# Performance work log

Measured on AMD Instinct MI355X. Metric: run time of the kernel, lower is better.

The kernel has to match this reference:

```python
import jax, jax.numpy as jnp
import numpy as np

N, E, H = 4096, 32768, 8
D0, C1, C2, C3 = 256, 448, 384, 256
K, M, G = 4, 500, 2000
NEG = 0.2   # GATConv LeakyReLU negative slope
EPS = 1e-5  # LayerNorm eps


def _gat(x, src, dst, W, a_s, a_d, b, heads, out_ch, concat):
    # PyG GATConv (self-loops already appended to src/dst by caller).
    n = x.shape[0]
    xp = (x @ W).reshape(n, heads, out_ch)                 # [N,H,C]
    s = jnp.einsum('nhc,hc->nh', xp, a_s)                  # alpha_src per node
    d = jnp.einsum('nhc,hc->nh', xp, a_d)                  # alpha_dst per node
    e = jax.nn.leaky_relu(s[src] + d[dst], NEG)            # [E,H]
    m = jax.ops.segment_max(e, dst, num_segments=n)
    m = jnp.where(jnp.isfinite(m), m, 0.0)
    p = jnp.exp(e - m[dst])
    z = jax.ops.segment_sum(p, dst, num_segments=n)
    alpha = p / (z[dst] + 1e-16)                           # per-dst softmax
    out = jax.ops.segment_sum(alpha[:, :, None] * xp[src], dst, num_segments=n)
    out = out.reshape(n, heads * out_ch) if concat else out[:, 0, :]
    return out + b


def _ln(x, g, b):
    mu = x.mean(-1, keepdims=True)
    v = ((x - mu) ** 2).mean(-1, keepdims=True)
    return (x - mu) * jax.lax.rsqrt(v + EPS) * g + b


def setup_inputs() -> dict:
    key = jax.random.key(0)
    ks = jax.random.split(key, 20)
    sc = 0.05
    inp = {
        'x': jax.random.normal(ks[0], (N, D0), jnp.float32),
        'edge_index': jax.random.randint(ks[1], (2, E), 0, N, jnp.int32),
        'W1': jax.random.normal(ks[2], (D0, H * C1), jnp.float32) * sc,
        'as1': jax.random.normal(ks[3], (H, C1), jnp.float32) * sc,
        'ad1': jax.random.normal(ks[4], (H, C1), jnp.float32) * sc,
        'b1': jnp.zeros((H * C1,), jnp.float32),
        'g1': jnp.ones((H * C1,), jnp.float32),
        'be1': jnp.zeros((H * C1,), jnp.float32),
        'W2': jax.random.normal(ks[5], (H * C1, H * C2), jnp.float32) * sc,
        'as2': jax.random.normal(ks[6], (H, C2), jnp.float32) * sc,
        'ad2': jax.random.normal(ks[7], (H, C2), jnp.float32) * sc,
        'b2': jnp.zeros((H * C2,), jnp.float32),
        'g2': jnp.ones((H * C2,), jnp.float32),
        'be2': jnp.zeros((H * C2,), jnp.float32),
        'W3': jax.random.normal(ks[8], (H * C2, H * C3), jnp.float32) * sc,
        'as3': jax.random.normal(ks[9], (H, C3), jnp.float32) * sc,
        'ad3': jax.random.normal(ks[10], (H, C3), jnp.float32) * sc,
        'b3': jnp.zeros((H * C3,), jnp.float32),
        'g3': jnp.ones((H * C3,), jnp.float32),
        'be3': jnp.zeros((H * C3,), jnp.float32),
        'Wh': jax.random.normal(ks[11], (K, H * C3, M), jnp.float32) * sc,
        'ash': jax.random.normal(ks[12], (K, 1, M), jnp.float32) * sc,
        'adh': jax.random.normal(ks[13], (K, 1, M), jnp.float32) * sc,
        'bh': jnp.zeros((K, M), jnp.float32),
        'idx': jnp.arange(G, dtype=jnp.int32).reshape(K, M),
    }
    return inp


def reference(x, edge_index, W1, as1, ad1, b1, g1, be1, W2, as2, ad2, b2, g2, be2,
              W3, as3, ad3, b3, g3, be3, Wh, ash, adh, bh, idx):
    n = x.shape[0]
    # eval mode: dropout_edge is identity; PyG GATConv adds self-loops
    loops = jnp.arange(n, dtype=edge_index.dtype)
    src = jnp.concatenate([edge_index[0], loops])
    dst = jnp.concatenate([edge_index[1], loops])

    h = jax.nn.relu(_gat(x, src, dst, W1, as1, ad1, b1, H, C1, True))
    h = _ln(h, g1, be1)
    h = jax.nn.relu(_gat(h, src, dst, W2, as2, ad2, b2, H, C2, True))
    h = _ln(h, g2, be2)
    h = jax.nn.relu(_gat(h, src, dst, W3, as3, ad3, b3, H, C3, True))
    h = _ln(h, g3, be3)

    per_head = jax.vmap(
        lambda Wk, ak_s, ak_d, bk: _gat(h, src, dst, Wk, ak_s, ak_d, bk, 1, M, False)
    )(Wh, ash, adh, bh)                                    # [K,N,M]

    vals = per_head.transpose(1, 0, 2).reshape(n, K * M)   # [N, G] in head order
    full = jnp.zeros((n, G), vals.dtype).at[:, idx.reshape(-1)].set(vals)
    return full, per_head
```

## Files before the change

### kernel.cpp

```cpp
#include <hip/hip_runtime.h>

#define NN 4096
#define EE 32768
#define ETOT (EE + NN)
#define HH 8
#define KK 4
#define MM 500
#define GG 2000
#define NEGS 0.2f
#define LNEPS 1e-5f

typedef unsigned short ushort;
typedef _Float16 half_t;
typedef __attribute__((ext_vector_type(8))) _Float16 half8;
typedef __attribute__((ext_vector_type(4))) float floatx4;


__device__ __forceinline__ void get_edge(const int* __restrict__ ei, int e, int& s, int& d) {
    if (e < EE) { s = ei[e]; d = ei[EE + e]; }
    else        { s = e - EE; d = e - EE; }
}

__device__ __forceinline__ void atomicMaxF(float* addr, float val) {
    if (val >= 0.f) atomicMax((int*)addr, __float_as_int(val));
    else            atomicMin((unsigned int*)addr, __float_as_uint(val));
}

__device__ __forceinline__ half_t f2h(float x) { return (half_t)x; }

__device__ __forceinline__ void async_lds16(const half_t* g, half_t* l) {
    __builtin_amdgcn_global_load_lds(
        (const __attribute__((address_space(1))) unsigned int*)(const void*)g,
        (__attribute__((address_space(3))) unsigned int*)(void*)l,
        16, 0, 0);
}


__global__ void k_zero_i(int* p, int n) {
    int i = blockIdx.x * 256 + threadIdx.x;
    if (i < n) p[i] = 0;
}

__global__ void k_zero_f(float* p, int n) {
    int i = blockIdx.x * 256 + threadIdx.x;
    if (i < n) p[i] = 0.f;
}

__global__ void k_count(const int* __restrict__ ei, int* deg) {
    int e = blockIdx.x * 256 + threadIdx.x;
    if (e < ETOT) { int s, d; get_edge(ei, e, s, d); atomicAdd(&deg[d], 1); }
}

__global__ void k_scan(const int* __restrict__ deg, int* rs, int n) {
    __shared__ int sums[1024];
    int tid = threadIdx.x;
    int base = tid * 4;
    int loc[4]; int s = 0;
    #pragma unroll
    for (int i = 0; i < 4; i++) {
        int v = (base + i < n) ? deg[base + i] : 0;
        loc[i] = s; s += v;
    }
    sums[tid] = s;
    __syncthreads();
    for (int off = 1; off < 1024; off <<= 1) {
        int v = (tid >= off) ? sums[tid - off] : 0;
        __syncthreads();
        sums[tid] += v;
        __syncthreads();
    }
    int prev = (tid > 0) ? sums[tid - 1] : 0;
    #pragma unroll
    for (int i = 0; i < 4; i++)
        if (base + i < n) rs[base + i] = prev + loc[i];
    if (tid == 1023) rs[n] = sums[1023];
}

__global__ void k_fill(const int* __restrict__ ei, const int* __restrict__ rs,
                       int* cur, int* csr_src, int* csr_eid) {
    int e = blockIdx.x * 256 + threadIdx.x;
    if (e < ETOT) {
        int s, d; get_edge(ei, e, s, d);
        int pos = rs[d] + atomicAdd(&cur[d], 1);
        csr_src[pos] = s;
        csr_eid[pos] = e;
    }
}


__global__ void k_f2h(const float* __restrict__ in, half_t* __restrict__ out, int n) {
    int i = blockIdx.x * 256 + threadIdx.x;
    if (i < n) out[i] = f2h(in[i]);
}


__global__ __launch_bounds__(256) void k_wt(const float* __restrict__ W,
                                            half_t* __restrict__ Wt,
                                            int Kd, int Nvalid, int ldw,
                                            long long sW, long long sWt) {
    __shared__ float t[32][33];
    const float* Wp = W + (size_t)blockIdx.z * sW;
    half_t* Wtp = Wt + (size_t)blockIdx.z * sWt;
    int n0 = blockIdx.x * 32, k0 = blockIdx.y * 32;
    int tx = threadIdx.x & 31, ty = threadIdx.x >> 5;
    #pragma unroll
    for (int i = 0; i < 32; i += 8)
        t[ty + i][tx] = (n0 + tx < Nvalid) ? Wp[(size_t)(k0 + ty + i) * ldw + n0 + tx] : 0.f;
    __syncthreads();
    #pragma unroll
    for (int i = 0; i < 32; i += 8)
        Wtp[(size_t)(n0 + ty + i) * Kd + k0 + tx] = f2h(t[tx][ty + i]);
}


#define BM 128
#define BN 128
#define BK 64

__global__ __launch_bounds__(256) void k_gemm_mfma(
    const half_t* __restrict__ A,
    const half_t* __restrict__ Bt,
    half_t* __restrict__ C,
    int Kd, int Nreal, int ldc,
    long long strideBt, long long strideC)
{
    __shared__ __align__(16) half_t As[BM * BK];
    __shared__ __align__(16) half_t Bs[BN * BK];

    const half_t* Btp = Bt + (size_t)blockIdx.z * strideBt;
    half_t* Cp = C + (size_t)blockIdx.z * strideC;
    int col0 = blockIdx.x * BN, row0 = blockIdx.y * BM;

    int lane = threadIdx.x & 63;
    int wave = threadIdx.x >> 6;
    int wm = (wave >> 1) * 64, wn = (wave & 1) * 64;

    int srow = wave * 32 + (lane >> 3);
    int gchunk = (lane & 7) ^ ((lane >> 3) & 7);
    const half_t* ga = A   + (size_t)(row0 + srow) * Kd + gchunk * 8;
    const half_t* gb = Btp + (size_t)(col0 + srow) * Kd + gchunk * 8;
    half_t* lA = &As[(wave * 32) * BK];
    half_t* lB = &Bs[(wave * 32) * BK];

    int r = lane & 15;
    int rx = r & 7;

    floatx4 acc[4][4];
    #pragma unroll
    for (int i = 0; i < 4; i++)
        #pragma unroll
        for (int j = 0; j < 4; j++) acc[i][j] = (floatx4){0.f, 0.f, 0.f, 0.f};

    for (int k0 = 0; k0 < Kd; k0 += BK) {
        #pragma unroll
        for (int j = 0; j < 4; j++) {
            async_lds16(ga + k0 + (size_t)(j * 8) * Kd, lA + (j * 8) * BK);
            async_lds16(gb + k0 + (size_t)(j * 8) * Kd, lB + (j * 8) * BK);
        }
        __syncthreads();
        #pragma unroll
        for (int kk = 0; kk < BK; kk += 32) {
            int phys = (((kk >> 3) + (lane >> 4)) ^ rx) << 3;
            half8 a[4], b[4];
            #pragma unroll
            for (int i = 0; i < 4; i++)
                a[i] = *(const half8*)&As[(wm + i * 16 + r) * BK + phys];
            #pragma unroll
            for (int j = 0; j < 4; j++)
                b[j] = *(const half8*)&Bs[(wn + j * 16 + r) * BK + phys];
            #pragma unroll
            for (int i = 0; i < 4; i++)
                #pragma unroll
                for (int j = 0; j < 4; j++)
                    acc[i][j] = __builtin_amdgcn_mfma_f32_16x16x32_f16(a[i], b[j], acc[i][j], 0, 0, 0);
        }
        __syncthreads();
    }

    int q4 = (lane >> 4) * 4;
    #pragma unroll
    for (int i = 0; i < 4; i++) {
        #pragma unroll
        for (int rr = 0; rr < 4; rr++) {
            int row = row0 + wm + i * 16 + q4 + rr;
            #pragma unroll
            for (int j = 0; j < 4; j++) {
                int col = col0 + wn + j * 16 + (lane & 15);
                if (col < Nreal) Cp[(size_t)row * ldc + col] = f2h(acc[i][j][rr]);
            }
        }
    }
}


__global__ void k_sd(const half_t* __restrict__ xp, const float* __restrict__ as_,
                     const float* __restrict__ ad_, float* s, float* d, int H, int C) {
    int n = blockIdx.x / H, h = blockIdx.x % H;
    int lane = threadIdx.x;
    const half_t* row = xp + (size_t)n * H * C + (size_t)h * C;
    const float* av = as_ + (size_t)h * C;
    const float* bv = ad_ + (size_t)h * C;
    float ss = 0.f, dd = 0.f;
    for (int c = lane; c < C; c += 64) {
        float x = (float)row[c];
        ss += x * av[c];
        dd += x * bv[c];
    }
    #pragma unroll
    for (int o = 32; o > 0; o >>= 1) {
        ss += __shfl_down(ss, o, 64);
        dd += __shfl_down(dd, o, 64);
    }
    if (lane == 0) { s[n * H + h] = ss; d[n * H + h] = dd; }
}


__global__ void k_init_mz(float* m, float* z, int n) {
    int i = blockIdx.x * 256 + threadIdx.x;
    if (i < n) { m[i] = -__builtin_inff(); z[i] = 0.f; }
}

__global__ void k_edge_max(const int* __restrict__ ei, const float* __restrict__ s,
                           const float* __restrict__ d, float* ew, float* m,
                           int H, int total) {
    int i = blockIdx.x * 256 + threadIdx.x;
    if (i >= total) return;
    int e = i / H, h = i - e * H;
    int sn, dn; get_edge(ei, e, sn, dn);
    float v = s[sn * H + h] + d[dn * H + h];
    v = (v >= 0.f) ? v : NEGS * v;
    ew[i] = v;
    atomicMaxF(&m[dn * H + h], v);
}

__global__ void k_edge_sum(const int* __restrict__ ei, float* ew,
                           const float* __restrict__ m, float* z, int H, int total) {
    int i = blockIdx.x * 256 + threadIdx.x;
    if (i >= total) return;
    int e = i / H, h = i - e * H;
    int sn, dn; get_edge(ei, e, sn, dn);
    float p = expf(ew[i] - m[dn * H + h]);
    ew[i] = p;
    atomicAdd(&z[dn * H + h], p);
}


__global__ __launch_bounds__(256) void k_agg_ln(
    const half_t* __restrict__ xp, const float* __restrict__ p, const float* __restrict__ z,
    const int* __restrict__ csr_src, const int* __restrict__ csr_eid,
    const int* __restrict__ rs, const float* __restrict__ bias,
    const float* __restrict__ gam, const float* __restrict__ bet,
    half_t* __restrict__ outh, int H, int C) {
    __shared__ int sh_src[256];
    __shared__ int sh_eid[256];
    __shared__ float sh_w[256 * HH];
    __shared__ float red[256];
    __shared__ float red2[256];
    int n = blockIdx.x, tid = threadIdx.x;
    int Dout = H * C;
    int NCH = Dout >> 3;
    int CCH = C >> 3;
    int start = rs[n], end = rs[n + 1];
    float acc[2][8];
    #pragma unroll
    for (int a = 0; a < 2; a++)
        #pragma unroll
        for (int e = 0; e < 8; e++) acc[a][e] = 0.f;

    for (int e0 = start; e0 < end; e0 += 256) {
        int cnt = min(256, end - e0);
        if (tid < cnt) { sh_src[tid] = csr_src[e0 + tid]; sh_eid[tid] = csr_eid[e0 + tid]; }
        __syncthreads();
        for (int i = tid; i < cnt * H; i += 256)
            sh_w[i] = p[sh_eid[i / H] * H + (i % H)];
        __syncthreads();
        int ai = 0;
        for (int ch = tid; ch < NCH; ch += 256, ai++) {
            int h = ch / CCH;
            float a0 = acc[ai][0], a1 = acc[ai][1], a2 = acc[ai][2], a3 = acc[ai][3];
            float a4 = acc[ai][4], a5 = acc[ai][5], a6 = acc[ai][6], a7 = acc[ai][7];
            for (int i = 0; i < cnt; i++) {
                float w = sh_w[i * H + h];
                half8 v = *(const half8*)(xp + (size_t)sh_src[i] * Dout + (ch << 3));
                a0 += w * (float)v[0]; a1 += w * (float)v[1];
                a2 += w * (float)v[2]; a3 += w * (float)v[3];
                a4 += w * (float)v[4]; a5 += w * (float)v[5];
                a6 += w * (float)v[6]; a7 += w * (float)v[7];
            }
            acc[ai][0] = a0; acc[ai][1] = a1; acc[ai][2] = a2; acc[ai][3] = a3;
            acc[ai][4] = a4; acc[ai][5] = a5; acc[ai][6] = a6; acc[ai][7] = a7;
        }
        __syncthreads();
    }

    float vals[2][8];
    float sum = 0.f, sumsq = 0.f;
    int ai = 0;
    for (int ch = tid; ch < NCH; ch += 256, ai++) {
        int h = ch / CCH;
        float zi = 1.f / (z[n * H + h] + 1e-16f);
        #pragma unroll
        for (int e = 0; e < 8; e++) {
            float v = acc[ai][e] * zi + bias[(ch << 3) + e];
            v = fmaxf(v, 0.f);
            vals[ai][e] = v;
            sum += v; sumsq += v * v;
        }
    }
    red[tid] = sum; red2[tid] = sumsq;
    __syncthreads();
    for (int o = 128; o > 0; o >>= 1) {
        if (tid < o) { red[tid] += red[tid + o]; red2[tid] += red2[tid + o]; }
        __syncthreads();
    }
    float mu = red[0] / Dout;
    float var = red2[0] / Dout - mu * mu;
    float rstd = rsqrtf(var + LNEPS);
    ai = 0;
    for (int ch = tid; ch < NCH; ch += 256, ai++) {
        half8 o;
        #pragma unroll
        for (int e = 0; e < 8; e++)
            o[e] = f2h((vals[ai][e] - mu) * rstd * gam[(ch << 3) + e] + bet[(ch << 3) + e]);
        *(half8*)(outh + (size_t)n * Dout + (ch << 3)) = o;
    }
}


__global__ __launch_bounds__(256) void k_agg_head(
    const half_t* __restrict__ xp, const float* __restrict__ p, const float* __restrict__ z,
    const int* __restrict__ csr_src, const int* __restrict__ csr_eid,
    const int* __restrict__ rs, const float* __restrict__ bias,
    const int* __restrict__ idxm, float* out_full, float* out_ph) {
    __shared__ int sh_src[256];
    __shared__ int sh_eid[256];
    __shared__ float sh_w[256 * KK];
    int n = blockIdx.x, tid = threadIdx.x;
    const int Dout = KK * MM;
    const int NCH = Dout >> 3;
    int start = rs[n], end = rs[n + 1];
    float acc[8];
    #pragma unroll
    for (int e = 0; e < 8; e++) acc[e] = 0.f;
    int ch = tid;
    int cb = ch << 3;

    for (int e0 = start; e0 < end; e0 += 256) {
        int cnt = min(256, end - e0);
        if (tid < cnt) { sh_src[tid] = csr_src[e0 + tid]; sh_eid[tid] = csr_eid[e0 + tid]; }
        __syncthreads();
        for (int i = tid; i < cnt * KK; i += 256)
            sh_w[i] = p[sh_eid[i / KK] * KK + (i % KK)];
        __syncthreads();
        if (ch < NCH) {
            for (int i = 0; i < cnt; i++) {
                const float* wv = &sh_w[i * KK];
                half8 v = *(const half8*)(xp + (size_t)sh_src[i] * Dout + cb);
                #pragma unroll
                for (int e = 0; e < 8; e++)
                    acc[e] += wv[(cb + e) / MM] * (float)v[e];
            }
        }
        __syncthreads();
    }
    if (ch < NCH) {
        #pragma unroll
        for (int e = 0; e < 8; e++) {
            int c = cb + e;
            int k = c / MM, m = c - k * MM;
            float v = acc[e] / (z[n * KK + k] + 1e-16f) + bias[c];
            out_ph[((size_t)k * NN + n) * MM + m] = v;
            out_full[(size_t)n * GG + idxm[c]] = v;
        }
    }
}


extern "C" void kernel_launch(void* const* d_in, const int* in_sizes, int n_in,
                              void* d_out, int out_size, void* d_ws, size_t ws_size,
                              hipStream_t stream) {
    (void)in_sizes; (void)n_in; (void)out_size; (void)ws_size;
    const float* x   = (const float*)d_in[0];
    const int*   ei  = (const int*)d_in[1];
    const float* W1  = (const float*)d_in[2];
    const float* as1 = (const float*)d_in[3];
    const float* ad1 = (const float*)d_in[4];
    const float* b1  = (const float*)d_in[5];
    const float* g1  = (const float*)d_in[6];
    const float* be1 = (const float*)d_in[7];
    const float* W2  = (const float*)d_in[8];
    const float* as2 = (const float*)d_in[9];
    const float* ad2 = (const float*)d_in[10];
    const float* b2  = (const float*)d_in[11];
    const float* g2  = (const float*)d_in[12];
    const float* be2 = (const float*)d_in[13];
    const float* W3  = (const float*)d_in[14];
    const float* as3 = (const float*)d_in[15];
    const float* ad3 = (const float*)d_in[16];
    const float* b3  = (const float*)d_in[17];
    const float* g3  = (const float*)d_in[18];
    const float* be3 = (const float*)d_in[19];
    const float* Wh  = (const float*)d_in[20];
    const float* ash = (const float*)d_in[21];
    const float* adh = (const float*)d_in[22];
    const float* bh  = (const float*)d_in[23];
    const int*   idxm = (const int*)d_in[24];
    float* out = (float*)d_out;

    char* w = (char*)d_ws;
    auto carve = [&](size_t bytes) { char* p = w; w += (bytes + 255) & ~(size_t)255; return p; };
    half_t* xp16    = (half_t*)carve((size_t)NN * 3584 * 2);
    half_t* Wt      = (half_t*)carve((size_t)3072 * 3584 * 2);
    float*  sarr    = (float*)carve((size_t)NN * HH * 4);
    float*  darr    = (float*)carve((size_t)NN * HH * 4);
    float*  marr    = (float*)carve((size_t)NN * HH * 4);
    float*  zarr    = (float*)carve((size_t)NN * HH * 4);
    float*  ework   = (float*)carve((size_t)ETOT * HH * 4);
    int*    csr_src = (int*)carve((size_t)ETOT * 4);
    int*    csr_eid = (int*)carve((size_t)ETOT * 4);
    int*    rowst   = (int*)carve((size_t)(NN + 1) * 4);
    int*    cur     = (int*)carve((size_t)NN * 4);
    half_t* Ah = (half_t*)d_out;

    k_zero_i<<<(NN + 255) / 256, 256, 0, stream>>>(cur, NN);
    k_count<<<(ETOT + 255) / 256, 256, 0, stream>>>(ei, cur);
    k_scan<<<1, 1024, 0, stream>>>(cur, rowst, NN);
    k_zero_i<<<(NN + 255) / 256, 256, 0, stream>>>(cur, NN);
    k_fill<<<(ETOT + 255) / 256, 256, 0, stream>>>(ei, rowst, cur, csr_src, csr_eid);

    k_f2h<<<(NN * 256 + 255) / 256, 256, 0, stream>>>(x, Ah, NN * 256);

    auto gat = [&](const float* W, const float* as_, const float* ad_,
                   const float* bias, const float* gam, const float* bet, int Din, int C) {
        int Dout = HH * C;
        k_wt<<<dim3(Dout / 32, Din / 32, 1), 256, 0, stream>>>(W, Wt, Din, Dout, Dout, 0, 0);
        k_gemm_mfma<<<dim3(Dout / BN, NN / BM, 1), 256, 0, stream>>>(
            Ah, Wt, xp16, Din, Dout, Dout, 0, 0);
        k_sd<<<NN * HH, 64, 0, stream>>>(xp16, as_, ad_, sarr, darr, HH, C);
        k_init_mz<<<(NN * HH + 255) / 256, 256, 0, stream>>>(marr, zarr, NN * HH);
        int tot = ETOT * HH;
        k_edge_max<<<(tot + 255) / 256, 256, 0, stream>>>(ei, sarr, darr, ework, marr, HH, tot);
        k_edge_sum<<<(tot + 255) / 256, 256, 0, stream>>>(ei, ework, marr, zarr, HH, tot);
        k_agg_ln<<<NN, 256, 0, stream>>>(xp16, ework, zarr, csr_src, csr_eid, rowst,
                                         bias, gam, bet, Ah, HH, C);
    };
    gat(W1, as1, ad1, b1, g1, be1, 256,  448);
    gat(W2, as2, ad2, b2, g2, be2, 3584, 384);
    gat(W3, as3, ad3, b3, g3, be3, 3072, 256);

    k_wt<<<dim3(512 / 32, 2048 / 32, KK), 256, 0, stream>>>(
        Wh, Wt, 2048, MM, MM, (long long)2048 * MM, (long long)512 * 2048);
    k_gemm_mfma<<<dim3(512 / BN, NN / BM, KK), 256, 0, stream>>>(
        Ah, Wt, xp16, 2048, MM, GG, (long long)512 * 2048, (long long)MM);
    k_sd<<<NN * KK, 64, 0, stream>>>(xp16, ash, adh, sarr, darr, KK, MM);
    k_init_mz<<<(NN * KK + 255) / 256, 256, 0, stream>>>(marr, zarr, NN * KK);
    int tot = ETOT * KK;
    k_edge_max<<<(tot + 255) / 256, 256, 0, stream>>>(ei, sarr, darr, ework, marr, KK, tot);
    k_edge_sum<<<(tot + 255) / 256, 256, 0, stream>>>(ei, ework, marr, zarr, KK, tot);
    k_zero_f<<<(NN * GG + 255) / 256, 256, 0, stream>>>(out, NN * GG);
    k_agg_head<<<NN, 256, 0, stream>>>(xp16, ework, zarr, csr_src, csr_eid, rowst,
                                       bh, idxm, out, out + (size_t)NN * GG);
}
```

Before: 725.4 us.

## Replace GEMM with 256x128 triple-buffered, 8-wave ping-pong MFMA kernel

The 128x128 single-buffer GEMM is replaced with a 256x128 tile kernel using 512 threads (8 waves). It keeps three LDS buffers so the async global-to-LDS loads for tile t+2 are issued while tile t is computed. Each K-step is split into two phases with explicit barriers, waitcnts, sched_barriers and setprio, so memory loads and MFMA bursts interleave across waves. The aim is to hide load latency and raise MFMA utilisation. In exchange, LDS use is higher (about 144KB), occupancy is lower, and the hand-tuned vmcnt counts must match the number of loads actually issued.

```diff
diff --git a/kernel.cpp b/kernel.cpp
--- a/kernel.cpp
+++ b/kernel.cpp
@@ -113,37 +113,36 @@
 }
 
 
-#define BM 128
-#define BN 128
-#define BK 64
-
-__global__ __launch_bounds__(256) void k_gemm_mfma(
+#define GBM 256
+#define GBN 128
+#define GBK 64
+
+__global__ __launch_bounds__(512, 2) void k_gemm_8ph(
     const half_t* __restrict__ A,
     const half_t* __restrict__ Bt,
     half_t* __restrict__ C,
     int Kd, int Nreal, int ldc,
     long long strideBt, long long strideC)
 {
-    __shared__ __align__(16) half_t As[BM * BK];
-    __shared__ __align__(16) half_t Bs[BN * BK];
+    __shared__ __align__(16) half_t As[3][GBM * GBK];
+    __shared__ __align__(16) half_t Bs[3][GBN * GBK];
 
     const half_t* Btp = Bt + (size_t)blockIdx.z * strideBt;
     half_t* Cp = C + (size_t)blockIdx.z * strideC;
-    int col0 = blockIdx.x * BN, row0 = blockIdx.y * BM;
-
-    int lane = threadIdx.x & 63;
-    int wave = threadIdx.x >> 6;
-    int wm = (wave >> 1) * 64, wn = (wave & 1) * 64;
-
-    int srow = wave * 32 + (lane >> 3);
-    int gchunk = (lane & 7) ^ ((lane >> 3) & 7);
-    const half_t* ga = A   + (size_t)(row0 + srow) * Kd + gchunk * 8;
-    const half_t* gb = Btp + (size_t)(col0 + srow) * Kd + gchunk * 8;
-    half_t* lA = &As[(wave * 32) * BK];
-    half_t* lB = &Bs[(wave * 32) * BK];
-
-    int r = lane & 15;
-    int rx = r & 7;
+    int col0 = blockIdx.x * GBN, row0 = blockIdx.y * GBM;
+
+    int l = threadIdx.x & 63;
+    int w = threadIdx.x >> 6;
+    int wm = (w >> 1) * 64, wn = (w & 1) * 64;
+
+    int lr = l >> 3, lc = l & 7;
+    int gch = lc ^ lr;
+    const half_t* gA = A   + (size_t)(row0 + w * 32 + lr) * Kd + gch * 8;
+    const half_t* gB = Btp + (size_t)(col0 + w * 16 + lr) * Kd + gch * 8;
+
+    int r = l & 15, rx = r & 7, qk = l >> 4;
+    int pa0 = ((0 + qk) ^ rx) << 3;
+    int pa1 = ((4 + qk) ^ rx) << 3;
 
     floatx4 acc[4][4];
     #pragma unroll
@@ -151,33 +150,89 @@
         #pragma unroll
         for (int j = 0; j < 4; j++) acc[i][j] = (floatx4){0.f, 0.f, 0.f, 0.f};
 
-    for (int k0 = 0; k0 < Kd; k0 += BK) {
-        #pragma unroll
-        for (int j = 0; j < 4; j++) {
-            async_lds16(ga + k0 + (size_t)(j * 8) * Kd, lA + (j * 8) * BK);
-            async_lds16(gb + k0 + (size_t)(j * 8) * Kd, lB + (j * 8) * BK);
-        }
-        __syncthreads();
-        #pragma unroll
-        for (int kk = 0; kk < BK; kk += 32) {
-            int phys = (((kk >> 3) + (lane >> 4)) ^ rx) << 3;
-            half8 a[4], b[4];
-            #pragma unroll
-            for (int i = 0; i < 4; i++)
-                a[i] = *(const half8*)&As[(wm + i * 16 + r) * BK + phys];
-            #pragma unroll
-            for (int j = 0; j < 4; j++)
-                b[j] = *(const half8*)&Bs[(wn + j * 16 + r) * BK + phys];
-            #pragma unroll
-            for (int i = 0; i < 4; i++)
-                #pragma unroll
-                for (int j = 0; j < 4; j++)
-                    acc[i][j] = __builtin_amdgcn_mfma_f32_16x16x32_f16(a[i], b[j], acc[i][j], 0, 0, 0);
-        }
-        __syncthreads();
-    }
-
-    int q4 = (lane >> 4) * 4;
+    int nt = Kd / GBK;
+
+    auto stageA = [&](int nb, int tt, int q) {
+        async_lds16(gA + (size_t)tt * GBK + (size_t)(q * 8) * Kd,
+                    &As[nb][(w * 32 + q * 8) * GBK]);
+    };
+    auto stageB = [&](int nb, int tt, int q) {
+        async_lds16(gB + (size_t)tt * GBK + (size_t)(q * 8) * Kd,
+                    &Bs[nb][(w * 16 + q * 8) * GBK]);
+    };
+
+    #pragma unroll
+    for (int q = 0; q < 4; q++) stageA(0, 0, q);
+    stageB(0, 0, 0); stageB(0, 0, 1);
+    #pragma unroll
+    for (int q = 0; q < 4; q++) stageA(1, 1, q);
+    stageB(1, 1, 0); stageB(1, 1, 1);
+    asm volatile("s_waitcnt vmcnt(6)" ::: "memory");
+    __builtin_amdgcn_s_barrier();
+    asm volatile("" ::: "memory");
+
+    int c = 0;
+    for (int t = 0; t < nt; ++t) {
+        int nb = c + 2; if (nb >= 3) nb -= 3;
+        bool st = (t + 2 < nt);
+        const half_t* Ar = &As[c][(wm + r) * GBK];
+        const half_t* Br = &Bs[c][(wn + r) * GBK];
+
+        half8 a[4][2], bA[2], bB[2];
+
+        #pragma unroll
+        for (int i = 0; i < 4; i++) {
+            a[i][0] = *(const half8*)(Ar + i * 16 * GBK + pa0);
+            a[i][1] = *(const half8*)(Ar + i * 16 * GBK + pa1);
+        }
+        bA[0] = *(const half8*)(Br + 0 * 16 * GBK + pa0);
+        bA[1] = *(const half8*)(Br + 0 * 16 * GBK + pa1);
+        bB[0] = *(const half8*)(Br + 1 * 16 * GBK + pa0);
+        bB[1] = *(const half8*)(Br + 1 * 16 * GBK + pa1);
+        if (st) { stageA(nb, t + 2, 0); stageA(nb, t + 2, 1); stageB(nb, t + 2, 0); }
+        __builtin_amdgcn_s_barrier();
+        asm volatile("s_waitcnt lgkmcnt(0)" ::: "memory");
+        __builtin_amdgcn_sched_barrier(0);
+        __builtin_amdgcn_s_setprio(1);
+        #pragma unroll
+        for (int i = 0; i < 4; i++) {
+            acc[i][0] = __builtin_amdgcn_mfma_f32_16x16x32_f16(a[i][0], bA[0], acc[i][0], 0, 0, 0);
+            acc[i][0] = __builtin_amdgcn_mfma_f32_16x16x32_f16(a[i][1], bA[1], acc[i][0], 0, 0, 0);
+            acc[i][1] = __builtin_amdgcn_mfma_f32_16x16x32_f16(a[i][0], bB[0], acc[i][1], 0, 0, 0);
+            acc[i][1] = __builtin_amdgcn_mfma_f32_16x16x32_f16(a[i][1], bB[1], acc[i][1], 0, 0, 0);
+        }
+        __builtin_amdgcn_s_setprio(0);
+        __builtin_amdgcn_sched_barrier(0);
+        __builtin_amdgcn_s_barrier();
+
+        bA[0] = *(const half8*)(Br + 2 * 16 * GBK + pa0);
+        bA[1] = *(const half8*)(Br + 2 * 16 * GBK + pa1);
+        bB[0] = *(const half8*)(Br + 3 * 16 * GBK + pa0);
+        bB[1] = *(const half8*)(Br + 3 * 16 * GBK + pa1);
+        if (st) { stageA(nb, t + 2, 2); stageA(nb, t + 2, 3); stageB(nb, t + 2, 1); }
+        if (st) asm volatile("s_waitcnt vmcnt(6)" ::: "memory");
+        else    asm volatile("s_waitcnt vmcnt(0)" ::: "memory");
+        __builtin_amdgcn_s_barrier();
+        asm volatile("" ::: "memory");
+        asm volatile("s_waitcnt lgkmcnt(0)" ::: "memory");
+        __builtin_amdgcn_sched_barrier(0);
+        __builtin_amdgcn_s_setprio(1);
+        #pragma unroll
+        for (int i = 0; i < 4; i++) {
+            acc[i][2] = __builtin_amdgcn_mfma_f32_16x16x32_f16(a[i][0], bA[0], acc[i][2], 0, 0, 0);
+            acc[i][2] = __builtin_amdgcn_mfma_f32_16x16x32_f16(a[i][1], bA[1], acc[i][2], 0, 0, 0);
+            acc[i][3] = __builtin_amdgcn_mfma_f32_16x16x32_f16(a[i][0], bB[0], acc[i][3], 0, 0, 0);
+            acc[i][3] = __builtin_amdgcn_mfma_f32_16x16x32_f16(a[i][1], bB[1], acc[i][3], 0, 0, 0);
+        }
+        __builtin_amdgcn_s_setprio(0);
+        __builtin_amdgcn_sched_barrier(0);
+        __builtin_amdgcn_s_barrier();
+        asm volatile("" ::: "memory");
+
+        c = (c == 2) ? 0 : c + 1;
+    }
+
+    int q4 = qk * 4;
     #pragma unroll
     for (int i = 0; i < 4; i++) {
         #pragma unroll
@@ -185,7 +240,7 @@
             int row = row0 + wm + i * 16 + q4 + rr;
             #pragma unroll
             for (int j = 0; j < 4; j++) {
-                int col = col0 + wn + j * 16 + (lane & 15);
+                int col = col0 + wn + j * 16 + r;
                 if (col < Nreal) Cp[(size_t)row * ldc + col] = f2h(acc[i][j][rr]);
             }
         }
@@ -434,7 +489,7 @@
                    const float* bias, const float* gam, const float* bet, int Din, int C) {
         int Dout = HH * C;
         k_wt<<<dim3(Dout / 32, Din / 32, 1), 256, 0, stream>>>(W, Wt, Din, Dout, Dout, 0, 0);
-        k_gemm_mfma<<<dim3(Dout / BN, NN / BM, 1), 256, 0, stream>>>(
+        k_gemm_8ph<<<dim3(Dout / GBN, NN / GBM, 1), 512, 0, stream>>>(
             Ah, Wt, xp16, Din, Dout, Dout, 0, 0);
         k_sd<<<NN * HH, 64, 0, stream>>>(xp16, as_, ad_, sarr, darr, HH, C);
         k_init_mz<<<(NN * HH + 255) / 256, 256, 0, stream>>>(marr, zarr, NN * HH);
@@ -450,7 +505,7 @@
 
     k_wt<<<dim3(512 / 32, 2048 / 32, KK), 256, 0, stream>>>(
         Wh, Wt, 2048, MM, MM, (long long)2048 * MM, (long long)512 * 2048);
-    k_gemm_mfma<<<dim3(512 / BN, NN / BM, KK), 256, 0, stream>>>(
+    k_gemm_8ph<<<dim3(512 / GBN, NN / GBM, KK), 512, 0, stream>>>(
         Ah, Wt, xp16, 2048, MM, GG, (long long)512 * 2048, (long long)MM);
     k_sd<<<NN * KK, 64, 0, stream>>>(xp16, ash, adh, sarr, darr, KK, MM);
     k_init_mz<<<(NN * KK + 255) / 256, 256, 0, stream>>>(marr, zarr, NN * KK);
```

After: 707.2 us. 1.03x faster.
